# Performance work log

Hardware: AMD Instinct MI355X
Metric: run time of the kernel (lower is better)

Reference implementation:

```python
import jax, jax.numpy as jnp
import numpy as np

WINDOW = 128  # window_size from init_kwargs
D = 1024      # input_dim
S = 8192      # seq_len


def setup_inputs() -> dict:
    key = jax.random.key(0)
    k1, k2, k3, k4, k5 = jax.random.split(key, 5)
    bound = 1.0 / np.sqrt(D)
    x = jax.random.normal(k1, (1, S, D), dtype=jnp.float32)
    Wq = jax.random.uniform(k2, (D, D), minval=-bound, maxval=bound, dtype=jnp.float32)
    bq = jax.random.uniform(k3, (D,), minval=-bound, maxval=bound, dtype=jnp.float32)
    Wk = jax.random.uniform(k4, (D, D), minval=-bound, maxval=bound, dtype=jnp.float32)
    bk = jax.random.uniform(k5, (D,), minval=-bound, maxval=bound, dtype=jnp.float32)
    return {"x": x, "Wq": Wq, "bq": bq, "Wk": Wk, "bk": bk}


def reference(x, Wq, bq, Wk, bk):
    # x: [1, S, D]  (original code only works with batch==1)
    xs = x[0]                          # [S, D]
    q = xs @ Wq.T + bq                 # [S, D]
    k = xs @ Wk.T + bk                 # [S, D]
    scores = q @ k.T                   # [S, S] dense, matches original buffer
    t = jnp.arange(S)[:, None]
    s = jnp.arange(S)[None, :]
    # original writes scores only for s in [t-WINDOW, t+WINDOW); elsewhere stays 0
    inwin = (s >= t - WINDOW) & (s < t + WINDOW)
    scores = jnp.where(inwin, scores, 0.0)
    attn = jax.nn.softmax(scores, axis=1)  # softmax INCLUDES the zero entries, as in original
    out = attn @ xs                    # [S, D]
    return out
```

## Files before the change

kernel.cpp:

```cpp
#include <hip/hip_runtime.h>

#define S 8192
#define D 1024
#define WINDOW 128
#define TQ 16
#define UMAX 288
#define BK 32
#define PAD 68
#define SCP 276
#define PP  296
#define NT  17

typedef __attribute__((ext_vector_type(8))) short short8;
typedef __attribute__((ext_vector_type(4))) float floatx4;
typedef __attribute__((ext_vector_type(4))) unsigned short ushort4v;
typedef unsigned short u16t;

__device__ __forceinline__ float wave_sum(float v) {
  #pragma unroll
  for (int off = 32; off > 0; off >>= 1) v += __shfl_xor(v, off, 64);
  return v;
}
__device__ __forceinline__ float wave_max(float v) {
  #pragma unroll
  for (int off = 32; off > 0; off >>= 1) v = fmaxf(v, __shfl_xor(v, off, 64));
  return v;
}
__device__ __forceinline__ unsigned int f2bf_rn(float f) {
  unsigned int u = __float_as_uint(f);
  return (u + 0x7fffu + ((u >> 16) & 1u)) >> 16;
}

__global__ __launch_bounds__(256) void split_kernel(
    const float* __restrict__ src, u16t* __restrict__ hi, u16t* __restrict__ lo)
{
  int i = (blockIdx.x * 256 + threadIdx.x) * 4;
  float4 v = *(const float4*)(src + i);
  float f[4] = {v.x, v.y, v.z, v.w};
  ushort4v h, l;
  #pragma unroll
  for (int c = 0; c < 4; ++c) {
    unsigned int hb = f2bf_rn(f[c]);
    float hf = __uint_as_float(hb << 16);
    unsigned int lb = f2bf_rn(f[c] - hf);
    h[c] = (u16t)hb;
    l[c] = (u16t)lb;
  }
  *(ushort4v*)(hi + i) = h;
  *(ushort4v*)(lo + i) = l;
}

__global__ __launch_bounds__(256) void transpose_x(const float* __restrict__ x,
                                                   u16t* __restrict__ xT)
{
  __shared__ float tile[64][65];
  const int s0 = blockIdx.x * 64;
  const int d0 = blockIdx.y * 64;
  const int t = threadIdx.x;
  #pragma unroll
  for (int p = 0; p < 4; ++p) {
    int r = (t >> 4) + p * 16;
    int c = (t & 15) * 4;
    float4 v = *(const float4*)(x + (size_t)(s0 + r) * D + d0 + c);
    tile[r][c+0] = v.x; tile[r][c+1] = v.y; tile[r][c+2] = v.z; tile[r][c+3] = v.w;
  }
  __syncthreads();
  #pragma unroll
  for (int p = 0; p < 4; ++p) {
    int dd = (t >> 4) + p * 16;
    int ss = (t & 15) * 4;
    ushort4v o;
    #pragma unroll
    for (int u = 0; u < 4; ++u) o[u] = (u16t)f2bf_rn(tile[ss + u][dd]);
    *(ushort4v*)(xT + (size_t)(d0 + dd) * S + s0 + ss) = o;
  }
}

__global__ __launch_bounds__(256) void gemm_qk(
    const u16t* __restrict__ xhi, const u16t* __restrict__ xlo,
    const u16t* __restrict__ wqhi, const u16t* __restrict__ wqlo,
    const u16t* __restrict__ wkhi, const u16t* __restrict__ wklo,
    const float* __restrict__ bqv, const float* __restrict__ bkv,
    u16t* __restrict__ qh, u16t* __restrict__ ql,
    u16t* __restrict__ kh, u16t* __restrict__ kl)
{
  __shared__ __align__(16) u16t Ah[128 * BK];
  __shared__ __align__(16) u16t Al[128 * BK];
  __shared__ __align__(16) u16t Bh[128 * BK];
  __shared__ __align__(16) u16t Bl[128 * BK];

  const int tid  = threadIdx.x;
  const int lane = tid & 63;
  const int wv   = tid >> 6;
  const int t0   = blockIdx.x * 128;
  const int n0   = blockIdx.y * 128;

  const u16t* whi = blockIdx.z ? wkhi : wqhi;
  const u16t* wlo = blockIdx.z ? wklo : wqlo;
  const float* bias = blockIdx.z ? bkv : bqv;
  u16t* oh = blockIdx.z ? kh : qh;
  u16t* ol = blockIdx.z ? kl : ql;

  floatx4 acc[4][4] = {};

  const int m0w  = (wv & 1) * 64;
  const int n0w  = (wv >> 1) * 64;
  const int srow = lane >> 2;
  const int scol = (lane & 3) * 8;

  for (int k0 = 0; k0 < D; k0 += BK) {
    __syncthreads();
    #pragma unroll
    for (int sg = 0; sg < 2; ++sg) {
      int seg  = wv * 2 + sg;
      int arow = t0 + seg * 16 + srow;
      int brow = n0 + seg * 16 + srow;
      size_t ga = (size_t)arow * D + k0 + scol;
      size_t gb = (size_t)brow * D + k0 + scol;
      __builtin_amdgcn_global_load_lds(
          (const __attribute__((address_space(1))) void*)(xhi + ga),
          (__attribute__((address_space(3))) void*)(&Ah[seg * 512]), 16, 0, 0);
      __builtin_amdgcn_global_load_lds(
          (const __attribute__((address_space(1))) void*)(xlo + ga),
          (__attribute__((address_space(3))) void*)(&Al[seg * 512]), 16, 0, 0);
      __builtin_amdgcn_global_load_lds(
          (const __attribute__((address_space(1))) void*)(whi + gb),
          (__attribute__((address_space(3))) void*)(&Bh[seg * 512]), 16, 0, 0);
      __builtin_amdgcn_global_load_lds(
          (const __attribute__((address_space(1))) void*)(wlo + gb),
          (__attribute__((address_space(3))) void*)(&Bl[seg * 512]), 16, 0, 0);
    }
    __syncthreads();

    short8 ah[4], al[4], bh[4], bl[4];
    #pragma unroll
    for (int t = 0; t < 4; ++t) {
      int ar = (m0w + t * 16 + (lane & 15)) * BK + (lane >> 4) * 8;
      int br = (n0w + t * 16 + (lane & 15)) * BK + (lane >> 4) * 8;
      ah[t] = *(const short8*)&Ah[ar];
      al[t] = *(const short8*)&Al[ar];
      bh[t] = *(const short8*)&Bh[br];
      bl[t] = *(const short8*)&Bl[br];
    }
    #pragma unroll
    for (int mt = 0; mt < 4; ++mt)
      #pragma unroll
      for (int nt = 0; nt < 4; ++nt) {
        acc[mt][nt] = __builtin_amdgcn_mfma_f32_16x16x32_bf16(ah[mt], bh[nt], acc[mt][nt], 0, 0, 0);
        acc[mt][nt] = __builtin_amdgcn_mfma_f32_16x16x32_bf16(ah[mt], bl[nt], acc[mt][nt], 0, 0, 0);
        acc[mt][nt] = __builtin_amdgcn_mfma_f32_16x16x32_bf16(al[mt], bh[nt], acc[mt][nt], 0, 0, 0);
      }
  }

  #pragma unroll
  for (int mt = 0; mt < 4; ++mt) {
    #pragma unroll
    for (int nt = 0; nt < 4; ++nt) {
      int n = n0 + n0w + nt * 16 + (lane & 15);
      int m = t0 + m0w + mt * 16 + (lane >> 4) * 4;
      float b = bias[n];
      #pragma unroll
      for (int r = 0; r < 4; ++r) {
        float v = acc[mt][nt][r] + b;
        unsigned int hb = f2bf_rn(v);
        float hf = __uint_as_float(hb << 16);
        unsigned int lb = f2bf_rn(v - hf);
        size_t idx = (size_t)(m + r) * D + n;
        oh[idx] = (u16t)hb;
        ol[idx] = (u16t)lb;
      }
    }
  }
}

__global__ __launch_bounds__(256) void colsum_kernel(const float* __restrict__ x,
                                                     float* __restrict__ xsum)
{
  int d = blockIdx.x * 256 + threadIdx.x;
  int tbase = blockIdx.y * 256;
  float s = 0.f;
  for (int t = 0; t < 256; ++t) s += x[(size_t)(tbase + t) * D + d];
  atomicAdd(&xsum[d], s);
}

__global__ __launch_bounds__(512) void attn_mfma(
    const u16t* __restrict__ qh_g, const u16t* __restrict__ ql_g,
    const u16t* __restrict__ kh_g, const u16t* __restrict__ kl_g,
    const u16t* __restrict__ xT, const float* __restrict__ xsum,
    float* __restrict__ out)
{
  __shared__ __align__(16) unsigned char lds[65088];
  u16t* kbuf = (u16t*)lds;
  u16t* qbh  = (u16t*)(lds + 22528);
  u16t* qbl  = (u16t*)(lds + 24576);
  u16t* XtL  = (u16t*)(lds);
  float* sc  = (float*)(lds + 37888);
  u16t* Pt   = (u16t*)(lds + 55552);
  float* e0d = (float*)(lds + 65024);

  const int tid  = threadIdx.x;
  const int lane = tid & 63;
  const int w    = tid >> 6;
  int bxs = (int)blockIdx.x;
  bxs = (bxs & 7) * 64 + (bxs >> 3);
  const int t0   = bxs * TQ;
  const int lo_u = max(0, t0 - WINDOW);
  const int hi_u = min(S, t0 + TQ - 1 + WINDOW);
  const int ucnt = hi_u - lo_u;

  for (int i = tid; i < 16 * SCP; i += 512) sc[i] = 0.f;
  for (int i = tid; i < 16 * PP; i += 512) Pt[i] = 0;

  floatx4 accS[3] = {};

  for (int d0 = 0; d0 < D; d0 += 32) {
    __syncthreads();
    for (int j = w; j < 22; j += 8) {
      int lg = j * 64 + lane;
      int row = lg / 5;
      int part = lg - row * 5; if (part > 3) part = 3;
      int rg = lo_u + row; if (rg > S - 1) rg = S - 1;
      const u16t* g = kh_g + ((size_t)rg << 10) + d0 + part * 8;
      __builtin_amdgcn_global_load_lds(
          (const __attribute__((address_space(1))) void*)g,
          (__attribute__((address_space(3))) void*)((unsigned char*)kbuf + j * 1024), 16, 0, 0);
    }
    if (w >= 6) {
      const u16t* src = (w == 6) ? qh_g : ql_g;
      u16t* dst = (w == 6) ? qbh : qbl;
      for (int j = 0; j < 2; ++j) {
        int lg = j * 64 + lane;
        int r0 = lg / 5;
        int part = lg - r0 * 5; if (part > 3) part = 3;
        int row = r0 > 15 ? 15 : r0;
        const u16t* g = src + ((size_t)(t0 + row) << 10) + d0 + part * 8;
        __builtin_amdgcn_global_load_lds(
            (const __attribute__((address_space(1))) void*)g,
            (__attribute__((address_space(3))) void*)((unsigned char*)dst + j * 1024), 16, 0, 0);
      }
    }
    __syncthreads();
    short8 aqh = *(const short8*)((unsigned char*)qbh + (lane & 15) * 80 + (lane >> 4) * 16);
    short8 aql = *(const short8*)((unsigned char*)qbl + (lane & 15) * 80 + (lane >> 4) * 16);
    #pragma unroll
    for (int i = 0; i < 3; ++i) {
      int tl = w + 8 * i;
      if (tl >= NT) continue;
      short8 kb = *(const short8*)((unsigned char*)kbuf + (tl * 16 + (lane & 15)) * 80 + (lane >> 4) * 16);
      accS[i] = __builtin_amdgcn_mfma_f32_16x16x32_bf16(aqh, kb, accS[i], 0, 0, 0);
      accS[i] = __builtin_amdgcn_mfma_f32_16x16x32_bf16(aql, kb, accS[i], 0, 0, 0);
    }
  }

  for (int d0 = 0; d0 < D; d0 += 32) {
    __syncthreads();
    for (int j = w; j < 22; j += 8) {
      int lg = j * 64 + lane;
      int row = lg / 5;
      int part = lg - row * 5; if (part > 3) part = 3;
      int rg = lo_u + row; if (rg > S - 1) rg = S - 1;
      const u16t* g = kl_g + ((size_t)rg << 10) + d0 + part * 8;
      __builtin_amdgcn_global_load_lds(
          (const __attribute__((address_space(1))) void*)g,
          (__attribute__((address_space(3))) void*)((unsigned char*)kbuf + j * 1024), 16, 0, 0);
    }
    if (w == 6) {
      for (int j = 0; j < 2; ++j) {
        int lg = j * 64 + lane;
        int r0 = lg / 5;
        int part = lg - r0 * 5; if (part > 3) part = 3;
        int row = r0 > 15 ? 15 : r0;
        const u16t* g = qh_g + ((size_t)(t0 + row) << 10) + d0 + part * 8;
        __builtin_amdgcn_global_load_lds(
            (const __attribute__((address_space(1))) void*)g,
            (__attribute__((address_space(3))) void*)((unsigned char*)qbh + j * 1024), 16, 0, 0);
      }
    }
    __syncthreads();
    short8 aqh = *(const short8*)((unsigned char*)qbh + (lane & 15) * 80 + (lane >> 4) * 16);
    #pragma unroll
    for (int i = 0; i < 3; ++i) {
      int tl = w + 8 * i;
      if (tl >= NT) continue;
      short8 kb = *(const short8*)((unsigned char*)kbuf + (tl * 16 + (lane & 15)) * 80 + (lane >> 4) * 16);
      accS[i] = __builtin_amdgcn_mfma_f32_16x16x32_bf16(aqh, kb, accS[i], 0, 0, 0);
    }
  }
  __syncthreads();

  {
    const int n_loc = lane & 15;
    #pragma unroll
    for (int i = 0; i < 3; ++i) {
      int tl = w + 8 * i;
      if (tl >= NT) continue;
      int s_loc = tl * 16 + n_loc;
      int s_g = lo_u + s_loc;
      #pragma unroll
      for (int r = 0; r < 4; ++r) {
        int m = (lane >> 4) * 4 + r;
        int t = t0 + m;
        if (s_g >= t - WINDOW && s_g < t + WINDOW && s_g < S)
          sc[m * SCP + s_loc] = accS[i][r];
      }
    }
  }
  __syncthreads();

  #pragma unroll
  for (int g = 0; g < 2; ++g) {
    int m = w * 2 + g;
    int t = t0 + m;
    int lo = max(0, t - WINDOW), hi = min(S, t + WINDOW);
    int cnt = hi - lo, off = lo - lo_u;
    float mx = 0.f;
    for (int i = lane; i < cnt; i += 64) mx = fmaxf(mx, sc[m * SCP + off + i]);
    mx = wave_max(mx);
    float e0 = __expf(-mx);
    float ss = 0.f;
    for (int i = lane; i < cnt; i += 64) ss += __expf(sc[m * SCP + off + i] - mx);
    ss = wave_sum(ss);
    float dinv = 1.f / (ss + (float)(S - cnt) * e0);
    for (int i = lane; i < cnt; i += 64) {
      float e = __expf(sc[m * SCP + off + i] - mx);
      Pt[m * PP + off + i] = (u16t)f2bf_rn((e - e0) * dinv);
    }
    if (lane == 0) e0d[m] = e0 * dinv;
  }

  for (int d0 = 0; d0 < D; d0 += 64) {
    __syncthreads();
    for (int j = w; j < 37; j += 8) {
      int lg = j * 64 + lane;
      int row = lg / 37;
      int chunk = lg - row * 37;
      int cg = lo_u + chunk * 8; if (cg > S - 8) cg = S - 8;
      const u16t* g = xT + (((size_t)(d0 + row)) << 13) + cg;
      __builtin_amdgcn_global_load_lds(
          (const __attribute__((address_space(1))) void*)g,
          (__attribute__((address_space(3))) void*)((unsigned char*)XtL + j * 1024), 16, 0, 0);
    }
    __syncthreads();
    if (w < 4) {
      floatx4 accO = {0.f, 0.f, 0.f, 0.f};
      #pragma unroll
      for (int c = 0; c < 9; ++c) {
        short8 pf = *(const short8*)((unsigned char*)Pt + (lane & 15) * (PP * 2) + c * 64 + (lane >> 4) * 16);
        short8 xf = *(const short8*)((unsigned char*)XtL + (w * 16 + (lane & 15)) * (PP * 2) + c * 64 + (lane >> 4) * 16);
        accO = __builtin_amdgcn_mfma_f32_16x16x32_bf16(pf, xf, accO, 0, 0, 0);
      }
      int n_g = d0 + w * 16 + (lane & 15);
      float xs = xsum[n_g];
      #pragma unroll
      for (int r = 0; r < 4; ++r) {
        int m = (lane >> 4) * 4 + r;
        out[(size_t)(t0 + m) * D + n_g] = accO[r] + e0d[m] * xs;
      }
    }
  }
}

__global__ __launch_bounds__(256) void proj_kernel(
    const float* __restrict__ x, const float* __restrict__ Wq,
    const float* __restrict__ bqv, const float* __restrict__ Wk,
    const float* __restrict__ bkv, float* __restrict__ qout,
    float* __restrict__ kout)
{
  __shared__ __align__(16) float xs[BK][PAD];
  __shared__ __align__(16) float wqs[BK][PAD];
  __shared__ __align__(16) float wks[BK][PAD];
  const int tid = threadIdx.x;
  const int tx = tid & 15, ty = tid >> 4;
  const int t0 = blockIdx.x * 64, i0 = blockIdx.y * 64;
  float accq[4][4] = {}, acck[4][4] = {};
  const int lrow0 = tid >> 3, lc4 = (tid & 7) * 4;
  for (int k0 = 0; k0 < D; k0 += BK) {
    __syncthreads();
    #pragma unroll
    for (int p = 0; p < 2; ++p) {
      int row = lrow0 + p * 32;
      float4 a = *(const float4*)(x  + (size_t)(t0 + row) * D + k0 + lc4);
      float4 b = *(const float4*)(Wq + (size_t)(i0 + row) * D + k0 + lc4);
      float4 c = *(const float4*)(Wk + (size_t)(i0 + row) * D + k0 + lc4);
      xs [lc4+0][row]=a.x; xs [lc4+1][row]=a.y; xs [lc4+2][row]=a.z; xs [lc4+3][row]=a.w;
      wqs[lc4+0][row]=b.x; wqs[lc4+1][row]=b.y; wqs[lc4+2][row]=b.z; wqs[lc4+3][row]=b.w;
      wks[lc4+0][row]=c.x; wks[lc4+1][row]=c.y; wks[lc4+2][row]=c.z; wks[lc4+3][row]=c.w;
    }
    __syncthreads();
    #pragma unroll
    for (int kk = 0; kk < BK; ++kk) {
      float4 av = *(const float4*)&xs [kk][ty*4];
      float4 bv = *(const float4*)&wqs[kk][tx*4];
      float4 cv = *(const float4*)&wks[kk][tx*4];
      float a[4] = {av.x, av.y, av.z, av.w};
      float b[4] = {bv.x, bv.y, bv.z, bv.w};
      float c[4] = {cv.x, cv.y, cv.z, cv.w};
      #pragma unroll
      for (int r = 0; r < 4; ++r)
        #pragma unroll
        for (int cc = 0; cc < 4; ++cc) {
          accq[r][cc] = fmaf(a[r], b[cc], accq[r][cc]);
          acck[r][cc] = fmaf(a[r], c[cc], acck[r][cc]);
        }
    }
  }
  float4 bq4 = *(const float4*)(bqv + i0 + tx*4);
  float4 bk4 = *(const float4*)(bkv + i0 + tx*4);
  #pragma unroll
  for (int r = 0; r < 4; ++r) {
    int trow = t0 + ty*4 + r;
    float4 oq = { accq[r][0]+bq4.x, accq[r][1]+bq4.y, accq[r][2]+bq4.z, accq[r][3]+bq4.w };
    float4 ok = { acck[r][0]+bk4.x, acck[r][1]+bk4.y, acck[r][2]+bk4.z, acck[r][3]+bk4.w };
    *(float4*)(qout + (size_t)trow * D + i0 + tx*4) = oq;
    *(float4*)(kout + (size_t)trow * D + i0 + tx*4) = ok;
  }
}

__global__ __launch_bounds__(256) void attn_kernel(
    const float* __restrict__ x, const float* __restrict__ q,
    const float* __restrict__ kmat, const float* __restrict__ xsum,
    float* __restrict__ out)
{
  __shared__ __align__(16) float scl[TQ][UMAX];
  __shared__ float e0s[TQ], dinv[TQ];
  const int tid = threadIdx.x, lane = tid & 63, wv = tid >> 6;
  const int t0 = blockIdx.x * TQ;
  const int lo_u = max(0, t0 - WINDOW);
  const int hi_u = min(S, t0 + TQ - 1 + WINDOW);
  const int ucnt = hi_u - lo_u;
  for (int i = tid; i < TQ * UMAX; i += 256) (&scl[0][0])[i] = 0.f;
  __syncthreads();
  {
    const int tiB = wv * 4;
    float4 qf[4][4];
    #pragma unroll
    for (int g = 0; g < 4; ++g) {
      int t = t0 + tiB + g;
      #pragma unroll
      for (int j = 0; j < 4; ++j)
        qf[g][j] = *(const float4*)(q + (size_t)t * D + lane*4 + j*256);
    }
    const int wlo = max(0, t0 + tiB - WINDOW);
    const int whi = min(S, t0 + tiB + 3 + WINDOW);
    for (int s = wlo; s < whi; ++s) {
      float4 kf[4];
      #pragma unroll
      for (int j = 0; j < 4; ++j)
        kf[j] = *(const float4*)(kmat + (size_t)s * D + lane*4 + j*256);
      float acc[4];
      #pragma unroll
      for (int g = 0; g < 4; ++g) {
        float v = 0.f;
        #pragma unroll
        for (int j = 0; j < 4; ++j) {
          v = fmaf(qf[g][j].x, kf[j].x, v);
          v = fmaf(qf[g][j].y, kf[j].y, v);
          v = fmaf(qf[g][j].z, kf[j].z, v);
          v = fmaf(qf[g][j].w, kf[j].w, v);
        }
        acc[g] = v;
      }
      #pragma unroll
      for (int g = 0; g < 4; ++g) {
        float tot = wave_sum(acc[g]);
        int t = t0 + tiB + g;
        if (lane == 0 && s >= t - WINDOW && s < t + WINDOW)
          scl[tiB + g][s - lo_u] = tot;
      }
    }
  }
  __syncthreads();
  #pragma unroll
  for (int g = 0; g < 4; ++g) {
    int ti = wv * 4 + g;
    int t = t0 + ti;
    int lo = max(0, t - WINDOW), hi = min(S, t + WINDOW);
    int cnt = hi - lo, off = lo - lo_u;
    float m = 0.f;
    for (int i = lane; i < cnt; i += 64) m = fmaxf(m, scl[ti][off + i]);
    m = wave_max(m);
    float e0 = __expf(-m);
    float ssum = 0.f;
    for (int i = lane; i < cnt; i += 64) {
      float e = __expf(scl[ti][off + i] - m);
      ssum += e;
      scl[ti][off + i] = e - e0;
    }
    ssum = wave_sum(ssum);
    if (lane == 0) {
      dinv[ti] = 1.f / (ssum + (float)(S - cnt) * e0);
      e0s[ti] = e0;
    }
  }
  __syncthreads();
  {
    const int c4 = tid * 4;
    float4 acc[TQ];
    #pragma unroll
    for (int ti = 0; ti < TQ; ++ti) acc[ti] = make_float4(0.f, 0.f, 0.f, 0.f);
    for (int su = 0; su < ucnt; su += 4) {
      float4 xr[4];
      #pragma unroll
      for (int u = 0; u < 4; ++u)
        xr[u] = *(const float4*)(x + (size_t)(lo_u + su + u) * D + c4);
      #pragma unroll
      for (int ti = 0; ti < TQ; ++ti) {
        float4 w4 = *(const float4*)&scl[ti][su];
        float wvv[4] = {w4.x, w4.y, w4.z, w4.w};
        #pragma unroll
        for (int u = 0; u < 4; ++u) {
          acc[ti].x = fmaf(wvv[u], xr[u].x, acc[ti].x);
          acc[ti].y = fmaf(wvv[u], xr[u].y, acc[ti].y);
          acc[ti].z = fmaf(wvv[u], xr[u].z, acc[ti].z);
          acc[ti].w = fmaf(wvv[u], xr[u].w, acc[ti].w);
        }
      }
    }
    float4 xsv = *(const float4*)(xsum + c4);
    #pragma unroll
    for (int ti = 0; ti < TQ; ++ti) {
      float e0 = e0s[ti], di = dinv[ti];
      float4 o;
      o.x = (acc[ti].x + e0 * xsv.x) * di;
      o.y = (acc[ti].y + e0 * xsv.y) * di;
      o.z = (acc[ti].z + e0 * xsv.z) * di;
      o.w = (acc[ti].w + e0 * xsv.w) * di;
      *(float4*)(out + (size_t)(t0 + ti) * D + c4) = o;
    }
  }
}

extern "C" void kernel_launch(void* const* d_in, const int* in_sizes, int n_in,
                              void* d_out, int out_size, void* d_ws, size_t ws_size,
                              hipStream_t stream) {
  const float* x  = (const float*)d_in[0];
  const float* Wq = (const float*)d_in[1];
  const float* bq = (const float*)d_in[2];
  const float* Wk = (const float*)d_in[3];
  const float* bk = (const float*)d_in[4];
  float* outp = (float*)d_out;

  const size_t SD = (size_t)S * D;
  const size_t DD = (size_t)D * D;

  float* xsum = (float*)d_ws;
  u16t* xhi = (u16t*)(xsum + D);
  u16t* xlo = xhi + SD;
  u16t* wqh = xlo + SD;
  u16t* wql = wqh + DD;
  u16t* wkh = wql + DD;
  u16t* wkl = wkh + DD;
  u16t* qh  = wkl + DD;
  u16t* ql  = qh + SD;
  u16t* kh  = ql + SD;
  u16t* kl  = kh + SD;
  u16t* xT  = kl + SD;
  size_t needed = (size_t)((char*)(xT + SD) - (char*)d_ws);

  hipMemsetAsync(xsum, 0, D * sizeof(float), stream);
  colsum_kernel<<<dim3(D / 256, S / 256), 256, 0, stream>>>(x, xsum);

  if (ws_size >= needed) {
    split_kernel<<<SD / 1024, 256, 0, stream>>>(x,  xhi, xlo);
    split_kernel<<<DD / 1024, 256, 0, stream>>>(Wq, wqh, wql);
    split_kernel<<<DD / 1024, 256, 0, stream>>>(Wk, wkh, wkl);
    transpose_x<<<dim3(S / 64, D / 64), 256, 0, stream>>>(x, xT);
    gemm_qk<<<dim3(S / 128, D / 128, 2), 256, 0, stream>>>(
        xhi, xlo, wqh, wql, wkh, wkl, bq, bk, qh, ql, kh, kl);
    attn_mfma<<<S / TQ, 512, 0, stream>>>(qh, ql, kh, kl, xT, xsum, outp);
  } else {
    float* q    = (float*)(xsum + D);
    float* kbuf = q + SD;
    proj_kernel<<<dim3(S / 64, D / 64), 256, 0, stream>>>(x, Wq, bq, Wk, bk, q, kbuf);
    attn_kernel<<<S / TQ, 256, 0, stream>>>(x, q, kbuf, xsum, outp);
  }
}
```

Before: 306.4 us.

## Split fused windowed attention into banded scores GEMM, softmax, and PV GEMM kernels

Replaces the monolithic per-16-row attention kernel with three kernels. A 128x128-tiled MFMA GEMM computes a 384-wide score band per 128 query rows. A row-wise softmax kernel then turns that band into bf16 probabilities, and a tiled MFMA GEMM multiplies those by transposed x. The aim is to remove the heavy redundant K and x reloads of the small 16-row tiles and to use larger, better-reused MFMA tiles. An XOR swizzle is also added to the LDS layout in gemm_qk and the new GEMMs to reduce bank conflicts. The cost is extra global round-trips for the fp32 band and the bf16 probability buffer, and 384 rather than about 272 columns of work per row.

Measured after the change: 297.0 us. 1.03x faster.

```diff
diff --git a/kernel.cpp b/kernel.cpp
--- a/kernel.cpp
+++ b/kernel.cpp
@@ -7,9 +7,7 @@
 #define UMAX 288
 #define BK 32
 #define PAD 68
-#define SCP 276
-#define PP  296
-#define NT  17
+#define BAND 384
 
 typedef __attribute__((ext_vector_type(8))) short short8;
 typedef __attribute__((ext_vector_type(4))) float floatx4;
@@ -106,7 +104,8 @@
   const int m0w  = (wv & 1) * 64;
   const int n0w  = (wv >> 1) * 64;
   const int srow = lane >> 2;
-  const int scol = (lane & 3) * 8;
+  const int scol = (((lane & 3) ^ ((lane >> 3) & 3))) * 8;
+  const int p8   = (((lane >> 4) ^ ((lane >> 1) & 3))) * 8;
 
   for (int k0 = 0; k0 < D; k0 += BK) {
     __syncthreads();
@@ -135,8 +134,8 @@
     short8 ah[4], al[4], bh[4], bl[4];
     #pragma unroll
     for (int t = 0; t < 4; ++t) {
-      int ar = (m0w + t * 16 + (lane & 15)) * BK + (lane >> 4) * 8;
-      int br = (n0w + t * 16 + (lane & 15)) * BK + (lane >> 4) * 8;
+      int ar = (m0w + t * 16 + (lane & 15)) * BK + p8;
+      int br = (n0w + t * 16 + (lane & 15)) * BK + p8;
       ah[t] = *(const short8*)&Ah[ar];
       al[t] = *(const short8*)&Al[ar];
       bh[t] = *(const short8*)&Bh[br];
@@ -183,178 +182,192 @@
   atomicAdd(&xsum[d], s);
 }
 
-__global__ __launch_bounds__(512) void attn_mfma(
-    const u16t* __restrict__ qh_g, const u16t* __restrict__ ql_g,
-    const u16t* __restrict__ kh_g, const u16t* __restrict__ kl_g,
-    const u16t* __restrict__ xT, const float* __restrict__ xsum,
-    float* __restrict__ out)
-{
-  __shared__ __align__(16) unsigned char lds[65088];
-  u16t* kbuf = (u16t*)lds;
-  u16t* qbh  = (u16t*)(lds + 22528);
-  u16t* qbl  = (u16t*)(lds + 24576);
-  u16t* XtL  = (u16t*)(lds);
-  float* sc  = (float*)(lds + 37888);
-  u16t* Pt   = (u16t*)(lds + 55552);
-  float* e0d = (float*)(lds + 65024);
+__global__ __launch_bounds__(256) void scores_kernel(
+    const u16t* __restrict__ qh, const u16t* __restrict__ ql,
+    const u16t* __restrict__ kh, const u16t* __restrict__ kl,
+    float* __restrict__ band)
+{
+  __shared__ __align__(16) u16t Ah[128 * BK];
+  __shared__ __align__(16) u16t Al[128 * BK];
+  __shared__ __align__(16) u16t Bh[128 * BK];
+  __shared__ __align__(16) u16t Bl[128 * BK];
 
   const int tid  = threadIdx.x;
   const int lane = tid & 63;
-  const int w    = tid >> 6;
-  int bxs = (int)blockIdx.x;
-  bxs = (bxs & 7) * 64 + (bxs >> 3);
-  const int t0   = bxs * TQ;
-  const int lo_u = max(0, t0 - WINDOW);
-  const int hi_u = min(S, t0 + TQ - 1 + WINDOW);
-  const int ucnt = hi_u - lo_u;
-
-  for (int i = tid; i < 16 * SCP; i += 512) sc[i] = 0.f;
-  for (int i = tid; i < 16 * PP; i += 512) Pt[i] = 0;
-
-  floatx4 accS[3] = {};
-
-  for (int d0 = 0; d0 < D; d0 += 32) {
-    __syncthreads();
-    for (int j = w; j < 22; j += 8) {
-      int lg = j * 64 + lane;
-      int row = lg / 5;
-      int part = lg - row * 5; if (part > 3) part = 3;
-      int rg = lo_u + row; if (rg > S - 1) rg = S - 1;
-      const u16t* g = kh_g + ((size_t)rg << 10) + d0 + part * 8;
-      __builtin_amdgcn_global_load_lds(
-          (const __attribute__((address_space(1))) void*)g,
-          (__attribute__((address_space(3))) void*)((unsigned char*)kbuf + j * 1024), 16, 0, 0);
-    }
-    if (w >= 6) {
-      const u16t* src = (w == 6) ? qh_g : ql_g;
-      u16t* dst = (w == 6) ? qbh : qbl;
-      for (int j = 0; j < 2; ++j) {
-        int lg = j * 64 + lane;
-        int r0 = lg / 5;
-        int part = lg - r0 * 5; if (part > 3) part = 3;
-        int row = r0 > 15 ? 15 : r0;
-        const u16t* g = src + ((size_t)(t0 + row) << 10) + d0 + part * 8;
-        __builtin_amdgcn_global_load_lds(
-            (const __attribute__((address_space(1))) void*)g,
-            (__attribute__((address_space(3))) void*)((unsigned char*)dst + j * 1024), 16, 0, 0);
-      }
-    }
-    __syncthreads();
-    short8 aqh = *(const short8*)((unsigned char*)qbh + (lane & 15) * 80 + (lane >> 4) * 16);
-    short8 aql = *(const short8*)((unsigned char*)qbl + (lane & 15) * 80 + (lane >> 4) * 16);
-    #pragma unroll
-    for (int i = 0; i < 3; ++i) {
-      int tl = w + 8 * i;
-      if (tl >= NT) continue;
-      short8 kb = *(const short8*)((unsigned char*)kbuf + (tl * 16 + (lane & 15)) * 80 + (lane >> 4) * 16);
-      accS[i] = __builtin_amdgcn_mfma_f32_16x16x32_bf16(aqh, kb, accS[i], 0, 0, 0);
-      accS[i] = __builtin_amdgcn_mfma_f32_16x16x32_bf16(aql, kb, accS[i], 0, 0, 0);
-    }
-  }
-
-  for (int d0 = 0; d0 < D; d0 += 32) {
-    __syncthreads();
-    for (int j = w; j < 22; j += 8) {
-      int lg = j * 64 + lane;
-      int row = lg / 5;
-      int part = lg - row * 5; if (part > 3) part = 3;
-      int rg = lo_u + row; if (rg > S - 1) rg = S - 1;
-      const u16t* g = kl_g + ((size_t)rg << 10) + d0 + part * 8;
-      __builtin_amdgcn_global_load_lds(
-          (const __attribute__((address_space(1))) void*)g,
-          (__attribute__((address_space(3))) void*)((unsigned char*)kbuf + j * 1024), 16, 0, 0);
-    }
-    if (w == 6) {
-      for (int j = 0; j < 2; ++j) {
-        int lg = j * 64 + lane;
-        int r0 = lg / 5;
-        int part = lg - r0 * 5; if (part > 3) part = 3;
-        int row = r0 > 15 ? 15 : r0;
-        const u16t* g = qh_g + ((size_t)(t0 + row) << 10) + d0 + part * 8;
-        __builtin_amdgcn_global_load_lds(
-            (const __attribute__((address_space(1))) void*)g,
-            (__attribute__((address_space(3))) void*)((unsigned char*)qbh + j * 1024), 16, 0, 0);
-      }
-    }
-    __syncthreads();
-    short8 aqh = *(const short8*)((unsigned char*)qbh + (lane & 15) * 80 + (lane >> 4) * 16);
-    #pragma unroll
-    for (int i = 0; i < 3; ++i) {
-      int tl = w + 8 * i;
-      if (tl >= NT) continue;
-      short8 kb = *(const short8*)((unsigned char*)kbuf + (tl * 16 + (lane & 15)) * 80 + (lane >> 4) * 16);
-      accS[i] = __builtin_amdgcn_mfma_f32_16x16x32_bf16(aqh, kb, accS[i], 0, 0, 0);
-    }
-  }
-  __syncthreads();
-
-  {
-    const int n_loc = lane & 15;
-    #pragma unroll
-    for (int i = 0; i < 3; ++i) {
-      int tl = w + 8 * i;
-      if (tl >= NT) continue;
-      int s_loc = tl * 16 + n_loc;
-      int s_g = lo_u + s_loc;
+  const int wv   = tid >> 6;
+  const int t0   = blockIdx.x * 128;
+  const int jt   = blockIdx.y;
+  const int s_base = t0 - 128 + jt * 128;
+
+  floatx4 acc[4][4] = {};
+
+  const int m0w  = (wv & 1) * 64;
+  const int n0w  = (wv >> 1) * 64;
+  const int srow = lane >> 2;
+  const int scol = (((lane & 3) ^ ((lane >> 3) & 3))) * 8;
+  const int p8   = (((lane >> 4) ^ ((lane >> 1) & 3))) * 8;
+
+  for (int k0 = 0; k0 < D; k0 += BK) {
+    __syncthreads();
+    #pragma unroll
+    for (int sg = 0; sg < 2; ++sg) {
+      int seg  = wv * 2 + sg;
+      int arow = t0 + seg * 16 + srow;
+      int brow = s_base + seg * 16 + srow;
+      brow = min(max(brow, 0), S - 1);
+      size_t ga = (size_t)arow * D + k0 + scol;
+      size_t gb = (size_t)brow * D + k0 + scol;
+      __builtin_amdgcn_global_load_lds(
+          (const __attribute__((address_space(1))) void*)(qh + ga),
+          (__attribute__((address_space(3))) void*)(&Ah[seg * 512]), 16, 0, 0);
+      __builtin_amdgcn_global_load_lds(
+          (const __attribute__((address_space(1))) void*)(ql + ga),
+          (__attribute__((address_space(3))) void*)(&Al[seg * 512]), 16, 0, 0);
+      __builtin_amdgcn_global_load_lds(
+          (const __attribute__((address_space(1))) void*)(kh + gb),
+          (__attribute__((address_space(3))) void*)(&Bh[seg * 512]), 16, 0, 0);
+      __builtin_amdgcn_global_load_lds(
+          (const __attribute__((address_space(1))) void*)(kl + gb),
+          (__attribute__((address_space(3))) void*)(&Bl[seg * 512]), 16, 0, 0);
+    }
+    __syncthreads();
+
+    short8 ah[4], al[4], bh[4], bl[4];
+    #pragma unroll
+    for (int t = 0; t < 4; ++t) {
+      int ar = (m0w + t * 16 + (lane & 15)) * BK + p8;
+      int br = (n0w + t * 16 + (lane & 15)) * BK + p8;
+      ah[t] = *(const short8*)&Ah[ar];
+      al[t] = *(const short8*)&Al[ar];
+      bh[t] = *(const short8*)&Bh[br];
+      bl[t] = *(const short8*)&Bl[br];
+    }
+    #pragma unroll
+    for (int mt = 0; mt < 4; ++mt)
+      #pragma unroll
+      for (int nt = 0; nt < 4; ++nt) {
+        acc[mt][nt] = __builtin_amdgcn_mfma_f32_16x16x32_bf16(ah[mt], bh[nt], acc[mt][nt], 0, 0, 0);
+        acc[mt][nt] = __builtin_amdgcn_mfma_f32_16x16x32_bf16(ah[mt], bl[nt], acc[mt][nt], 0, 0, 0);
+        acc[mt][nt] = __builtin_amdgcn_mfma_f32_16x16x32_bf16(al[mt], bh[nt], acc[mt][nt], 0, 0, 0);
+      }
+  }
+
+  #pragma unroll
+  for (int mt = 0; mt < 4; ++mt) {
+    #pragma unroll
+    for (int nt = 0; nt < 4; ++nt) {
+      int n_loc = n0w + nt * 16 + (lane & 15);
+      int s = s_base + n_loc;
       #pragma unroll
       for (int r = 0; r < 4; ++r) {
-        int m = (lane >> 4) * 4 + r;
-        int t = t0 + m;
-        if (s_g >= t - WINDOW && s_g < t + WINDOW && s_g < S)
-          sc[m * SCP + s_loc] = accS[i][r];
-      }
-    }
-  }
-  __syncthreads();
-
-  #pragma unroll
-  for (int g = 0; g < 2; ++g) {
-    int m = w * 2 + g;
-    int t = t0 + m;
-    int lo = max(0, t - WINDOW), hi = min(S, t + WINDOW);
-    int cnt = hi - lo, off = lo - lo_u;
-    float mx = 0.f;
-    for (int i = lane; i < cnt; i += 64) mx = fmaxf(mx, sc[m * SCP + off + i]);
-    mx = wave_max(mx);
-    float e0 = __expf(-mx);
-    float ss = 0.f;
-    for (int i = lane; i < cnt; i += 64) ss += __expf(sc[m * SCP + off + i] - mx);
-    ss = wave_sum(ss);
-    float dinv = 1.f / (ss + (float)(S - cnt) * e0);
-    for (int i = lane; i < cnt; i += 64) {
-      float e = __expf(sc[m * SCP + off + i] - mx);
-      Pt[m * PP + off + i] = (u16t)f2bf_rn((e - e0) * dinv);
-    }
-    if (lane == 0) e0d[m] = e0 * dinv;
-  }
-
-  for (int d0 = 0; d0 < D; d0 += 64) {
-    __syncthreads();
-    for (int j = w; j < 37; j += 8) {
-      int lg = j * 64 + lane;
-      int row = lg / 37;
-      int chunk = lg - row * 37;
-      int cg = lo_u + chunk * 8; if (cg > S - 8) cg = S - 8;
-      const u16t* g = xT + (((size_t)(d0 + row)) << 13) + cg;
-      __builtin_amdgcn_global_load_lds(
-          (const __attribute__((address_space(1))) void*)g,
-          (__attribute__((address_space(3))) void*)((unsigned char*)XtL + j * 1024), 16, 0, 0);
-    }
-    __syncthreads();
-    if (w < 4) {
-      floatx4 accO = {0.f, 0.f, 0.f, 0.f};
-      #pragma unroll
-      for (int c = 0; c < 9; ++c) {
-        short8 pf = *(const short8*)((unsigned char*)Pt + (lane & 15) * (PP * 2) + c * 64 + (lane >> 4) * 16);
-        short8 xf = *(const short8*)((unsigned char*)XtL + (w * 16 + (lane & 15)) * (PP * 2) + c * 64 + (lane >> 4) * 16);
-        accO = __builtin_amdgcn_mfma_f32_16x16x32_bf16(pf, xf, accO, 0, 0, 0);
-      }
-      int n_g = d0 + w * 16 + (lane & 15);
+        int m_loc = m0w + mt * 16 + (lane >> 4) * 4 + r;
+        int t = t0 + m_loc;
+        bool inwin = (s >= t - WINDOW) && (s < t + WINDOW) && (s >= 0) && (s < S);
+        band[(size_t)t * BAND + jt * 128 + n_loc] = inwin ? acc[mt][nt][r] : 0.f;
+      }
+    }
+  }
+}
+
+__global__ __launch_bounds__(256) void softmax_kernel(
+    const float* __restrict__ band, u16t* __restrict__ Pb, float* __restrict__ e0d)
+{
+  const int lane = threadIdx.x & 63;
+  const int w    = threadIdx.x >> 6;
+  const int t    = blockIdx.x * 4 + w;
+  const float* row = band + (size_t)t * BAND;
+
+  float v[6];
+  float mx = 0.f;
+  #pragma unroll
+  for (int i = 0; i < 6; ++i) {
+    v[i] = row[i * 64 + lane];
+    mx = fmaxf(mx, v[i]);
+  }
+  mx = wave_max(mx);
+  float e0 = __expf(-mx);
+  float ss = 0.f;
+  #pragma unroll
+  for (int i = 0; i < 6; ++i) {
+    v[i] = __expf(v[i] - mx);
+    ss += v[i];
+  }
+  ss = wave_sum(ss);
+  float dinv = 1.f / (ss + (float)(S - BAND) * e0);
+  #pragma unroll
+  for (int i = 0; i < 6; ++i)
+    Pb[(size_t)t * BAND + i * 64 + lane] = (u16t)f2bf_rn((v[i] - e0) * dinv);
+  if (lane == 0) e0d[t] = e0 * dinv;
+}
+
+__global__ __launch_bounds__(256) void pv_kernel(
+    const u16t* __restrict__ Pb, const u16t* __restrict__ xT,
+    const float* __restrict__ e0d, const float* __restrict__ xsum,
+    float* __restrict__ out)
+{
+  __shared__ __align__(16) u16t Ab[128 * BK];
+  __shared__ __align__(16) u16t Bb[128 * BK];
+
+  const int tid  = threadIdx.x;
+  const int lane = tid & 63;
+  const int wv   = tid >> 6;
+  const int t0   = blockIdx.x * 128;
+  const int d0   = blockIdx.y * 128;
+  const int origin = t0 - 128;
+
+  floatx4 acc[4][4] = {};
+
+  const int m0w  = (wv & 1) * 64;
+  const int n0w  = (wv >> 1) * 64;
+  const int srow = lane >> 2;
+  const int scol = (((lane & 3) ^ ((lane >> 3) & 3))) * 8;
+  const int p8   = (((lane >> 4) ^ ((lane >> 1) & 3))) * 8;
+
+  for (int k0 = 0; k0 < BAND; k0 += BK) {
+    __syncthreads();
+    #pragma unroll
+    for (int sg = 0; sg < 2; ++sg) {
+      int seg  = wv * 2 + sg;
+      int arow = t0 + seg * 16 + srow;
+      int brow = d0 + seg * 16 + srow;
+      int s_g  = origin + k0 + scol;
+      s_g = min(max(s_g, 0), S - 8);
+      size_t ga = (size_t)arow * BAND + k0 + scol;
+      size_t gb = (size_t)brow * S + s_g;
+      __builtin_amdgcn_global_load_lds(
+          (const __attribute__((address_space(1))) void*)(Pb + ga),
+          (__attribute__((address_space(3))) void*)(&Ab[seg * 512]), 16, 0, 0);
+      __builtin_amdgcn_global_load_lds(
+          (const __attribute__((address_space(1))) void*)(xT + gb),
+          (__attribute__((address_space(3))) void*)(&Bb[seg * 512]), 16, 0, 0);
+    }
+    __syncthreads();
+
+    short8 af[4], bf[4];
+    #pragma unroll
+    for (int t = 0; t < 4; ++t) {
+      int ar = (m0w + t * 16 + (lane & 15)) * BK + p8;
+      int br = (n0w + t * 16 + (lane & 15)) * BK + p8;
+      af[t] = *(const short8*)&Ab[ar];
+      bf[t] = *(const short8*)&Bb[br];
+    }
+    #pragma unroll
+    for (int mt = 0; mt < 4; ++mt)
+      #pragma unroll
+      for (int nt = 0; nt < 4; ++nt)
+        acc[mt][nt] = __builtin_amdgcn_mfma_f32_16x16x32_bf16(af[mt], bf[nt], acc[mt][nt], 0, 0, 0);
+  }
+
+  #pragma unroll
+  for (int mt = 0; mt < 4; ++mt) {
+    #pragma unroll
+    for (int nt = 0; nt < 4; ++nt) {
+      int n_g = d0 + n0w + nt * 16 + (lane & 15);
       float xs = xsum[n_g];
       #pragma unroll
       for (int r = 0; r < 4; ++r) {
-        int m = (lane >> 4) * 4 + r;
-        out[(size_t)(t0 + m) * D + n_g] = accO[r] + e0d[m] * xs;
+        int m_g = t0 + m0w + mt * 16 + (lane >> 4) * 4 + r;
+        out[(size_t)m_g * D + n_g] = acc[mt][nt][r] + e0d[m_g] * xs;
       }
     }
   }
@@ -557,6 +570,10 @@
   u16t* xT  = kl + SD;
   size_t needed = (size_t)((char*)(xT + SD) - (char*)d_ws);
 
+  float* band = (float*)xhi;
+  u16t*  Pb   = xlo;
+  float* e0d  = (float*)(Pb + (size_t)S * BAND);
+
   hipMemsetAsync(xsum, 0, D * sizeof(float), stream);
   colsum_kernel<<<dim3(D / 256, S / 256), 256, 0, stream>>>(x, xsum);
 
@@ -567,7 +584,9 @@
     transpose_x<<<dim3(S / 64, D / 64), 256, 0, stream>>>(x, xT);
     gemm_qk<<<dim3(S / 128, D / 128, 2), 256, 0, stream>>>(
         xhi, xlo, wqh, wql, wkh, wkl, bq, bk, qh, ql, kh, kl);
-    attn_mfma<<<S / TQ, 512, 0, stream>>>(qh, ql, kh, kl, xT, xsum, outp);
+    scores_kernel<<<dim3(S / 128, 3), 256, 0, stream>>>(qh, ql, kh, kl, band);
+    softmax_kernel<<<S / 4, 256, 0, stream>>>(band, Pb, e0d);
+    pv_kernel<<<dim3(S / 128, D / 128), 256, 0, stream>>>(Pb, xT, e0d, xsum, outp);
   } else {
     float* q    = (float*)(xsum + D);
     float* kbuf = q + SD;
```
